# Performance work log

Hardware: AMD Instinct MI355X
Metric: run time of the kernel (lower is better)

## Reference

```python
import jax, jax.numpy as jnp
import numpy as np

B, S, D = 2, 2048, 4096
NH, NKV = 32, 8
HD = D // NH          # 128
NREP = NH // NKV      # 4 (GQA groups)


def _rope(t, cos, sin):
    # t: [b, s, h, d]; cos/sin: [s, d//2]; interleaved (real, imag) pairs on last dim
    tr = t.reshape(*t.shape[:-1], -1, 2)
    a, b = tr[..., 0], tr[..., 1]
    c = cos[None, :, None, :]
    s = sin[None, :, None, :]
    out = jnp.stack([a * c - b * s, a * s + b * c], axis=-1)
    return out.reshape(t.shape)


def _repeat_kv(t, n_rep):
    # [b, s, n_kv, d] -> [b, s, n_kv*n_rep, d]
    b, s, nkv, d = t.shape
    return jnp.broadcast_to(t[:, :, :, None, :], (b, s, nkv, n_rep, d)).reshape(b, s, nkv * n_rep, d)


def setup_inputs() -> dict:
    key = jax.random.key(0)
    ks = jax.random.split(key, 5)
    x = jax.random.normal(ks[0], (B, S, D), jnp.float32)
    wq = jax.random.normal(ks[1], (D, NH * HD), jnp.float32) * 0.02
    wk = jax.random.normal(ks[2], (D, NKV * HD), jnp.float32) * 0.02
    wv = jax.random.normal(ks[3], (D, NKV * HD), jnp.float32) * 0.02
    wo = jax.random.normal(ks[4], (NH * HD, D), jnp.float32) * 0.02
    inv_freq = 1.0 / (10000.0 ** (jnp.arange(0, HD, 2, dtype=jnp.float32) / HD))
    angles = jnp.arange(S, dtype=jnp.float32)[:, None] * inv_freq[None, :]  # [S, HD//2]
    return {
        "x": x, "wq": wq, "wk": wk, "wv": wv, "wo": wo,
        "freqs_cos": jnp.cos(angles), "freqs_sin": jnp.sin(angles),
        "start_pos": 0,
    }


def reference(x, wq, wk, wv, wo, freqs_cos, freqs_sin, start_pos):
    b, s, _ = x.shape
    xq = (x @ wq).reshape(b, s, NH, HD)
    xk = (x @ wk).reshape(b, s, NKV, HD)
    xv = (x @ wv).reshape(b, s, NKV, HD)
    xq = _rope(xq, freqs_cos, freqs_sin)
    xk = _rope(xk, freqs_cos, freqs_sin)
    # prefill (start_pos=0): cache[:b, :s] = xk/xv, then keys/values read back equal xk/xv
    keys = _repeat_kv(xk, NREP)    # [b, s, NH, HD]
    values = _repeat_kv(xv, NREP)  # [b, s, NH, HD]
    scores = jnp.einsum("bqhd,bkhd->bhqk", xq, keys) / jnp.sqrt(jnp.float32(HD))
    probs = jax.nn.softmax(scores, axis=-1)
    out = jnp.einsum("bhqk,bkhd->bqhd", probs, values).reshape(b, s, NH * HD)
    return out @ wo
```

## Files before the change

### kernel.cpp

```cpp
#include <hip/hip_runtime.h>
#include <hip/hip_bf16.h>
#include <cstdint>

#define B_   2
#define S_   2048
#define D_   4096
#define NH_  32
#define NKV_ 8
#define HD_  128
#define BS_  (B_*S_)
#define NQK_ 6144

typedef __bf16 bf16_t;
typedef __bf16 bf16x8 __attribute__((ext_vector_type(8)));
typedef __bf16 bf16x4 __attribute__((ext_vector_type(4)));
typedef __bf16 bf16x2 __attribute__((ext_vector_type(2)));
typedef float  f32x4  __attribute__((ext_vector_type(4)));
typedef unsigned uint32x4 __attribute__((ext_vector_type(4)));

typedef const __attribute__((address_space(1))) void* gas_ptr;
typedef __attribute__((address_space(3))) void* las_ptr;

__device__ __forceinline__ void gload_lds16(const void* g, void* l) {
  __builtin_amdgcn_global_load_lds((gas_ptr)g, (las_ptr)l, 16, 0, 0);
}

__device__ __forceinline__ float exp2_fast(float x) {
  float r;
  asm("v_exp_f32 %0, %1" : "=v"(r) : "v"(x));
  return r;
}

__device__ __forceinline__ unsigned cvt_pk_bf16(float a, float b) {
  unsigned r;
  asm("v_cvt_pk_bf16_f32 %0, %1, %2" : "=v"(r) : "v"(a), "v"(b));
  return r;
}

#define LD8(p) (*(const bf16x8*)(p))
#define MFMA(a, b, c) __builtin_amdgcn_mfma_f32_16x16x32_bf16(a, b, c, 0, 0, 0)

__global__ __launch_bounds__(256) void k_cvt(const float4* __restrict__ in,
                                             bf16x4* __restrict__ out, int n4) {
  int i = blockIdx.x * 256 + threadIdx.x;
  if (i >= n4) return;
  float4 v = in[i];
  bf16x4 o = { (bf16_t)v.x, (bf16_t)v.y, (bf16_t)v.z, (bf16_t)v.w };
  out[i] = o;
}

__global__ __launch_bounds__(256) void k_transpose_cvt(const float* __restrict__ w,
                                                       bf16_t* __restrict__ wt,
                                                       int K, int N) {
  __shared__ float tile[32][33];
  int n0 = blockIdx.x * 32, k0 = blockIdx.y * 32;
  int tx = threadIdx.x, ty = threadIdx.y;
#pragma unroll
  for (int i = 0; i < 4; i++)
    tile[ty + 8*i][tx] = w[(size_t)(k0 + ty + 8*i) * N + n0 + tx];
  __syncthreads();
#pragma unroll
  for (int i = 0; i < 4; i++)
    wt[(size_t)(n0 + ty + 8*i) * K + k0 + tx] = (bf16_t)tile[tx][ty + 8*i];
}

template <typename CT, int NF>
__global__ __launch_bounds__(512, 2) void k_gemm8p(const bf16_t* __restrict__ A,
                                                   const bf16_t* __restrict__ Bt,
                                                   CT* __restrict__ C,
                                                   int M, int N, int K) {
  __shared__ __align__(16) bf16_t As[2][256 * 64];
  __shared__ __align__(16) bf16_t Bs[2][NF * 64 * 64];
  const int tid = threadIdx.x;
  const int l = tid & 63, w = tid >> 6;
  const int lr = l & 15, lg = l >> 4;
  const int wm = w >> 2, wn = w & 3;

  const int bm = blockIdx.x, bn = blockIdx.y;

  const bf16_t* Ab = A  + (size_t)bm * 256 * K;
  const bf16_t* Bb = Bt + (size_t)bn * (NF * 64) * K;

  int st_row[4], st_col[4], st_dst[4];
#pragma unroll
  for (int j = 0; j < 4; j++) {
    int o = (j * 512 + tid) * 16;
    int row = o >> 7, cb = o & 127;
    st_row[j] = row;
    st_col[j] = (cb ^ ((row & 7) << 4)) >> 1;
    st_dst[j] = o >> 1;
  }

  int aoff[8], boff[NF];
#pragma unroll
  for (int m = 0; m < 8; m++) {
    int r = wm * 128 + m * 16 + lr;
    aoff[m] = r * 64 + (((lg * 16) ^ ((r & 7) << 4)) >> 1);
  }
#pragma unroll
  for (int n = 0; n < NF; n++) {
    int r = wn * (16 * NF) + n * 16 + lr;
    boff[n] = r * 64 + (((lg * 16) ^ ((r & 7) << 4)) >> 1);
  }

  f32x4 acc[8][NF];
#pragma unroll
  for (int m = 0; m < 8; m++)
#pragma unroll
    for (int n = 0; n < NF; n++) acc[m][n] = f32x4{0.f, 0.f, 0.f, 0.f};

  auto stageA = [&](int k, int h) {
    const int kt = k << 6;
    const int rof = h << 7;
#pragma unroll
    for (int j = 0; j < 2; j++)
      gload_lds16(Ab + (size_t)(st_row[j] + rof) * K + kt + st_col[j],
                  &As[k & 1][0] + (rof << 6) + st_dst[j]);
  };
  auto stageB = [&](int k) {
    const int kt = k << 6;
#pragma unroll
    for (int j = 0; j < NF; j++)
      gload_lds16(Bb + (size_t)st_row[j] * K + kt + st_col[j],
                  &Bs[k & 1][0] + st_dst[j]);
  };

  const int NT = K >> 6;
  stageA(0, 0); stageA(0, 1); stageB(0); stageB(1);
  if constexpr (NF == 3) asm volatile("s_waitcnt vmcnt(3)" ::: "memory");
  else                   asm volatile("s_waitcnt vmcnt(4)" ::: "memory");
  __builtin_amdgcn_s_barrier();

  for (int k = 0; k < NT; ++k) {
    const bf16_t* Ap = &As[k & 1][0];
    const bf16_t* Bp = &Bs[k & 1][0];
    const bool s1 = (k + 1 < NT), s2 = (k + 2 < NT);
    bf16x8 bfr[NF], a[4];

#pragma unroll
    for (int n = 0; n < NF; n++) bfr[n] = LD8(Bp + boff[n]);
#pragma unroll
    for (int m = 0; m < 4; m++) a[m] = LD8(Ap + aoff[m]);
    if (s1) stageA(k + 1, 0);
    __builtin_amdgcn_s_barrier();
    asm volatile("s_waitcnt lgkmcnt(0)" ::: "memory");
    __builtin_amdgcn_s_setprio(1);
#pragma unroll
    for (int m = 0; m < 4; m++)
#pragma unroll
      for (int n = 0; n < NF; n++)
        acc[m][n] = MFMA(a[m], bfr[n], acc[m][n]);
    __builtin_amdgcn_s_setprio(0);
    __builtin_amdgcn_s_barrier();

#pragma unroll
    for (int m = 0; m < 4; m++) a[m] = LD8(Ap + aoff[m + 4]);
    if (s1) stageA(k + 1, 1);
    __builtin_amdgcn_s_barrier();
    asm volatile("s_waitcnt lgkmcnt(0)" ::: "memory");
    __builtin_amdgcn_s_setprio(1);
#pragma unroll
    for (int m = 0; m < 4; m++)
#pragma unroll
      for (int n = 0; n < NF; n++)
        acc[m + 4][n] = MFMA(a[m], bfr[n], acc[m + 4][n]);
    __builtin_amdgcn_s_setprio(0);
    __builtin_amdgcn_s_barrier();

#pragma unroll
    for (int n = 0; n < NF; n++) bfr[n] = LD8(Bp + (boff[n] ^ 32));
#pragma unroll
    for (int m = 0; m < 4; m++) a[m] = LD8(Ap + (aoff[m] ^ 32));
    __builtin_amdgcn_s_barrier();
    asm volatile("s_waitcnt lgkmcnt(0)" ::: "memory");
    __builtin_amdgcn_s_setprio(1);
#pragma unroll
    for (int m = 0; m < 4; m++)
#pragma unroll
      for (int n = 0; n < NF; n++)
        acc[m][n] = MFMA(a[m], bfr[n], acc[m][n]);
    __builtin_amdgcn_s_setprio(0);
    __builtin_amdgcn_s_barrier();

#pragma unroll
    for (int m = 0; m < 4; m++) a[m] = LD8(Ap + (aoff[m + 4] ^ 32));
    if (s2) {
      stageB(k + 2);
      if constexpr (NF == 3) asm volatile("s_waitcnt vmcnt(3)" ::: "memory");
      else                   asm volatile("s_waitcnt vmcnt(4)" ::: "memory");
    } else if (s1) {
      asm volatile("s_waitcnt vmcnt(0)" ::: "memory");
    }
    __builtin_amdgcn_s_barrier();
    asm volatile("s_waitcnt lgkmcnt(0)" ::: "memory");
    __builtin_amdgcn_s_setprio(1);
#pragma unroll
    for (int m = 0; m < 4; m++)
#pragma unroll
      for (int n = 0; n < NF; n++)
        acc[m + 4][n] = MFMA(a[m], bfr[n], acc[m + 4][n]);
    __builtin_amdgcn_s_setprio(0);
    __builtin_amdgcn_s_barrier();
  }

#pragma unroll
  for (int m = 0; m < 8; m++) {
    int row0 = bm * 256 + wm * 128 + m * 16 + lg * 4;
#pragma unroll
    for (int n = 0; n < NF; n++) {
      int col = bn * (NF * 64) + wn * (16 * NF) + n * 16 + lr;
#pragma unroll
      for (int i = 0; i < 4; i++)
        C[(size_t)(row0 + i) * N + col] = (CT)acc[m][n][i];
    }
  }
}

__global__ __launch_bounds__(256) void k_rope(const bf16_t* __restrict__ qkv,
                                              const float* __restrict__ fcos,
                                              const float* __restrict__ fsin,
                                              bf16_t* __restrict__ dst,
                                              int nheads, int col_off, float mul) {
  int idx = blockIdx.x * 256 + threadIdx.x;
  int p = idx & 63;
  int h = (idx >> 6) % nheads;
  int bs = idx / (64 * nheads);
  int s = bs & (S_ - 1);
  int b = bs >> 11;
  const bf16_t* src = qkv + (size_t)bs * NQK_ + col_off + h * HD_ + 2 * p;
  bf16x2 ab = *(const bf16x2*)src;
  float a = (float)ab[0], bb = (float)ab[1];
  float c = fcos[s * 64 + p], sn = fsin[s * 64 + p];
  bf16x2 o = { (bf16_t)((a * c - bb * sn) * mul), (bf16_t)((a * sn + bb * c) * mul) };
  *(bf16x2*)(dst + ((((size_t)b * nheads + h) * S_ + s) * HD_) + 2 * p) = o;
}

__global__ __launch_bounds__(256) void k_vtrans(const bf16_t* __restrict__ qkv,
                                                bf16_t* __restrict__ vtr) {
  __shared__ bf16_t tile[32][33];
  int s0 = blockIdx.x * 32, d0 = blockIdx.y * 32, z = blockIdx.z;
  int b = z >> 3, kvh = z & 7;
  int tx = threadIdx.x, ty = threadIdx.y;
#pragma unroll
  for (int i = 0; i < 4; i++)
    tile[ty + 8*i][tx] =
        qkv[(size_t)(b * S_ + s0 + ty + 8*i) * NQK_ + (D_ + NKV_ * HD_) + kvh * HD_ + d0 + tx];
  __syncthreads();
#pragma unroll
  for (int i = 0; i < 4; i++)
    vtr[((size_t)z * HD_ + d0 + ty + 8*i) * S_ + s0 + tx] = tile[tx][ty + 8*i];
}

#define KVBLK 64
#define SM_THR 12.0f
__global__ __launch_bounds__(256, 2) void k_flash(const bf16_t* __restrict__ qr,
                                                  const bf16_t* __restrict__ kr,
                                                  const bf16_t* __restrict__ vt,
                                                  bf16_t* __restrict__ ctx) {
  __shared__ __align__(16) bf16_t Ks[2][KVBLK * HD_];
  __shared__ __align__(16) bf16_t Vs[2][HD_ * KVBLK];
  const int tid = threadIdx.x;
  const int l = tid & 63, w = tid >> 6;
  const int lr = l & 15, lg = l >> 4;
  const int qb = blockIdx.x, h = blockIdx.y, b = blockIdx.z;
  const int kvh = h >> 2;

  const bf16_t* qbase = qr + (((size_t)b * NH_ + h) * S_ + qb * 128 + w * 32) * HD_;
  const bf16_t* kbase = kr + (((size_t)b * NKV_ + kvh) * S_) * HD_;
  const bf16_t* vbase = vt + (((size_t)b * NKV_ + kvh) * HD_) * S_;

  const int sl0 = (lr + ((lg & 1) << 5)) << 2;
  const int sl1 = sl0 + (16 << 2);

  bf16x8 qf[2][4];
#pragma unroll
  for (int m = 0; m < 2; m++)
#pragma unroll
    for (int kk = 0; kk < 4; kk++)
      qf[m][kk] = *(const bf16x8*)(qbase + (m * 16 + lr) * HD_ + kk * 32 + lg * 8);

  bf16x8 ones;
#pragma unroll
  for (int j = 0; j < 8; j++) ones[j] = (bf16_t)1.0f;

  f32x4 o[2][9];
#pragma unroll
  for (int m = 0; m < 2; m++)
#pragma unroll
    for (int n = 0; n < 9; n++) o[m][n] = f32x4{0.f, 0.f, 0.f, 0.f};
  float mR[2] = {-1e30f, -1e30f};

  auto stage = [&](int bu, int t) {
    const int kb = t * KVBLK;
#pragma unroll
    for (int j = 0; j < 4; j++) {
      int o_ = (tid + 256 * j) * 16;
      int row = o_ >> 8, cb = o_ & 255;
      int scb = cb ^ ((row & 7) << 4);
      gload_lds16(kbase + (size_t)(kb + row) * HD_ + (scb >> 1),
                  &Ks[bu][0] + (o_ >> 1));
    }
#pragma unroll
    for (int j = 0; j < 4; j++) {
      int o_ = (tid + 256 * j) * 16;
      int row = o_ >> 7, cb = o_ & 127;
      int scb = cb ^ ((row & 7) << 4);
      gload_lds16(vbase + (size_t)row * S_ + kb + (scb >> 1),
                  &Vs[bu][0] + (o_ >> 1));
    }
  };

  const int nt = S_ / KVBLK;
  stage(0, 0);
  __syncthreads();
  int buf = 0;

  for (int t = 0; t < nt; t++) {
    if (t + 1 < nt) stage(buf ^ 1, t + 1);
    const bf16_t* Kb = &Ks[buf][0];
    const bf16_t* Vb = &Vs[buf][0];

    f32x4 sc[2][4];
#pragma unroll
    for (int m = 0; m < 2; m++)
#pragma unroll
      for (int n = 0; n < 4; n++) sc[m][n] = f32x4{0.f, 0.f, 0.f, 0.f};
    __builtin_amdgcn_s_setprio(1);
#pragma unroll
    for (int n = 0; n < 4; n++) {
#pragma unroll
      for (int kk = 0; kk < 4; kk++) {
        int r = n * 16 + lr;
        int cb = (kk * 64 + lg * 16) ^ ((r & 7) << 4);
        bf16x8 kf = *(const bf16x8*)(Kb + (((r << 8) + cb) >> 1));
        sc[0][n] = MFMA(kf, qf[0][kk], sc[0][n]);
        sc[1][n] = MFMA(kf, qf[1][kk], sc[1][n]);
      }
    }
    __builtin_amdgcn_s_setprio(0);

    bf16x8 pf[2][2];
#pragma unroll
    for (int m = 0; m < 2; m++) {
      float lm = sc[m][0][0];
#pragma unroll
      for (int n = 0; n < 4; n++)
#pragma unroll
        for (int i = 0; i < 4; i++)
          if (n | i) lm = fmaxf(lm, sc[m][n][i]);
      if (!__all(lm - mR[m] <= SM_THR)) {
        float tmx = fmaxf(lm, __shfl_xor(lm, 16));
        tmx = fmaxf(tmx, __shfl_xor(tmx, 32));
        float mnew = fmaxf(mR[m], tmx);
        float alpha = exp2_fast(mR[m] - mnew);
        mR[m] = mnew;
        float av[4];
#pragma unroll
        for (int i = 0; i < 4; i++) av[i] = __shfl(alpha, lg * 4 + i);
#pragma unroll
        for (int n = 0; n < 9; n++)
#pragma unroll
          for (int i = 0; i < 4; i++) o[m][n][i] *= av[i];
      }
      unsigned W[4][2];
#pragma unroll
      for (int n = 0; n < 4; n++) {
        float p0 = exp2_fast(sc[m][n][0] - mR[m]);
        float p1 = exp2_fast(sc[m][n][1] - mR[m]);
        float p2 = exp2_fast(sc[m][n][2] - mR[m]);
        float p3 = exp2_fast(sc[m][n][3] - mR[m]);
        W[n][0] = cvt_pk_bf16(p0, p1);
        W[n][1] = cvt_pk_bf16(p2, p3);
      }
#pragma unroll
      for (int kk = 0; kk < 2; kk++) {
        uint32x4 wv;
#pragma unroll
        for (int t = 0; t < 4; t++) {
          int srcb = (t < 2) ? sl0 : sl1;
          unsigned lo = (unsigned)__builtin_amdgcn_ds_bpermute(srcb, (int)W[2 * kk][t & 1]);
          unsigned hi = (unsigned)__builtin_amdgcn_ds_bpermute(srcb, (int)W[2 * kk + 1][t & 1]);
          wv[t] = (l & 32) ? hi : lo;
        }
        pf[m][kk] = __builtin_bit_cast(bf16x8, wv);
      }
    }

    __builtin_amdgcn_s_setprio(1);
#pragma unroll
    for (int n = 0; n < 8; n++) {
#pragma unroll
      for (int kk = 0; kk < 2; kk++) {
        int r = n * 16 + lr;
        int cb = (kk * 64 + lg * 16) ^ ((r & 7) << 4);
        bf16x8 vf = *(const bf16x8*)(Vb + (((r << 7) + cb) >> 1));
        o[0][n] = MFMA(pf[0][kk], vf, o[0][n]);
        o[1][n] = MFMA(pf[1][kk], vf, o[1][n]);
      }
    }
    o[0][8] = MFMA(pf[0][0], ones, o[0][8]);
    o[0][8] = MFMA(pf[0][1], ones, o[0][8]);
    o[1][8] = MFMA(pf[1][0], ones, o[1][8]);
    o[1][8] = MFMA(pf[1][1], ones, o[1][8]);
    __builtin_amdgcn_s_setprio(0);
    __syncthreads();
    buf ^= 1;
  }

#pragma unroll
  for (int m = 0; m < 2; m++)
#pragma unroll
    for (int i = 0; i < 4; i++) {
      float inv = 1.0f / o[m][8][i];
      int srow = qb * 128 + w * 32 + m * 16 + lg * 4 + i;
#pragma unroll
      for (int n = 0; n < 8; n++) {
        int d = n * 16 + lr;
        ctx[((size_t)(b * S_ + srow)) * D_ + h * HD_ + d] = (bf16_t)(o[m][n][i] * inv);
      }
    }
}

extern "C" void kernel_launch(void* const* d_in, const int* in_sizes, int n_in,
                              void* d_out, int out_size, void* d_ws, size_t ws_size,
                              hipStream_t stream) {
  const float* x    = (const float*)d_in[0];
  const float* wq   = (const float*)d_in[1];
  const float* wk   = (const float*)d_in[2];
  const float* wv   = (const float*)d_in[3];
  const float* wo   = (const float*)d_in[4];
  const float* fcos = (const float*)d_in[5];
  const float* fsin = (const float*)d_in[6];
  float* out = (float*)d_out;

  const size_t SZ_XB    = (size_t)BS_ * D_ * 2;
  const size_t SZ_WQKVT = (size_t)NQK_ * D_ * 2;
  const size_t SZ_WOT   = (size_t)D_ * D_ * 2;
  char* p = (char*)d_ws;
  bf16_t* xb    = (bf16_t*)p;
  bf16_t* wqkvt = (bf16_t*)(p + SZ_XB);
  bf16_t* wot   = (bf16_t*)(p + SZ_XB + SZ_WQKVT);
  bf16_t* qkv   = (bf16_t*)(p + SZ_XB + SZ_WQKVT + SZ_WOT);
  bf16_t* qrope = xb;
  bf16_t* krope = wqkvt;
  bf16_t* vtr   = wqkvt + (size_t)BS_ * NKV_ * HD_;
  bf16_t* ctx   = qkv;

  const float QSCALE = (float)(0.08838834764831845 * 1.4426950408889634);

  dim3 tb(32, 8);
  k_cvt<<<BS_ * D_ / 1024, 256, 0, stream>>>((const float4*)x, (bf16x4*)xb, BS_ * D_ / 4);
  k_transpose_cvt<<<dim3(D_ / 32, D_ / 32), tb, 0, stream>>>(wq, wqkvt, D_, D_);
  k_transpose_cvt<<<dim3(32, D_ / 32), tb, 0, stream>>>(wk, wqkvt + (size_t)D_ * D_, D_, NKV_ * HD_);
  k_transpose_cvt<<<dim3(32, D_ / 32), tb, 0, stream>>>(wv, wqkvt + (size_t)(D_ + NKV_ * HD_) * D_, D_, NKV_ * HD_);
  k_transpose_cvt<<<dim3(D_ / 32, D_ / 32), tb, 0, stream>>>(wo, wot, D_, D_);
  k_gemm8p<bf16_t, 3><<<dim3(BS_ / 256, NQK_ / 192), 512, 0, stream>>>(xb, wqkvt, qkv, BS_, NQK_, D_);
  k_rope<<<BS_ * NH_ * 64 / 256, 256, 0, stream>>>(qkv, fcos, fsin, qrope, NH_, 0, QSCALE);
  k_rope<<<BS_ * NKV_ * 64 / 256, 256, 0, stream>>>(qkv, fcos, fsin, krope, NKV_, D_, 1.0f);
  k_vtrans<<<dim3(S_ / 32, HD_ / 32, B_ * NKV_), tb, 0, stream>>>(qkv, vtr);
  k_flash<<<dim3(S_ / 128, NH_, B_), 256, 0, stream>>>(qrope, krope, vtr, ctx);
  k_gemm8p<float, 4><<<dim3(BS_ / 256, D_ / 256), 512, 0, stream>>>(ctx, wot, out, BS_, D_, D_);
}
```

Before: 606.0 us.

## Split QKV GEMM into Q GEMM and split-K KV GEMM with 256-wide tiles

The fused QKV projection with 192-wide N tiles becomes a Q-only GEMM plus a KV GEMM that uses split-K over two partial buffers. RoPE and V-transpose sum the two partials as they read them. The GEMM kernel now uses only the 256x256 (NF=4) tile. The intent is better tile efficiency and more blocks for the narrow KV part, since its 16x8 grid is too small to fill the GPU without split-K. In exchange it adds extra partial-buffer traffic and rounds the partial sums to bf16, and it reorders the wo transpose to reuse the workspace.

After: 575.1 us. 1.05x faster.

```diff
diff --git a/kernel.cpp b/kernel.cpp
--- a/kernel.cpp
+++ b/kernel.cpp
@@ -64,11 +64,13 @@
     wt[(size_t)(n0 + ty + 8*i) * K + k0 + tx] = (bf16_t)tile[tx][ty + 8*i];
 }
 
-template <typename CT, int NF>
+template <typename CT>
 __global__ __launch_bounds__(512, 2) void k_gemm8p(const bf16_t* __restrict__ A,
                                                    const bf16_t* __restrict__ Bt,
                                                    CT* __restrict__ C,
-                                                   int M, int N, int K) {
+                                                   int M, int N, int K, int KL,
+                                                   long long zsC) {
+  constexpr int NF = 4;
   __shared__ __align__(16) bf16_t As[2][256 * 64];
   __shared__ __align__(16) bf16_t Bs[2][NF * 64 * 64];
   const int tid = threadIdx.x;
@@ -77,9 +79,11 @@
   const int wm = w >> 2, wn = w & 3;
 
   const int bm = blockIdx.x, bn = blockIdx.y;
-
-  const bf16_t* Ab = A  + (size_t)bm * 256 * K;
-  const bf16_t* Bb = Bt + (size_t)bn * (NF * 64) * K;
+  const int kOff = blockIdx.z * KL;
+
+  const bf16_t* Ab = A  + (size_t)bm * 256 * K + kOff;
+  const bf16_t* Bb = Bt + (size_t)bn * 256 * K + kOff;
+  C += (long long)blockIdx.z * zsC;
 
   int st_row[4], st_col[4], st_dst[4];
 #pragma unroll
@@ -99,7 +103,7 @@
   }
 #pragma unroll
   for (int n = 0; n < NF; n++) {
-    int r = wn * (16 * NF) + n * 16 + lr;
+    int r = wn * 64 + n * 16 + lr;
     boff[n] = r * 64 + (((lg * 16) ^ ((r & 7) << 4)) >> 1);
   }
 
@@ -125,10 +129,9 @@
                   &Bs[k & 1][0] + st_dst[j]);
   };
 
-  const int NT = K >> 6;
+  const int NT = KL >> 6;
   stageA(0, 0); stageA(0, 1); stageB(0); stageB(1);
-  if constexpr (NF == 3) asm volatile("s_waitcnt vmcnt(3)" ::: "memory");
-  else                   asm volatile("s_waitcnt vmcnt(4)" ::: "memory");
+  asm volatile("s_waitcnt vmcnt(4)" ::: "memory");
   __builtin_amdgcn_s_barrier();
 
   for (int k = 0; k < NT; ++k) {
@@ -186,8 +189,7 @@
     for (int m = 0; m < 4; m++) a[m] = LD8(Ap + (aoff[m + 4] ^ 32));
     if (s2) {
       stageB(k + 2);
-      if constexpr (NF == 3) asm volatile("s_waitcnt vmcnt(3)" ::: "memory");
-      else                   asm volatile("s_waitcnt vmcnt(4)" ::: "memory");
+      asm volatile("s_waitcnt vmcnt(4)" ::: "memory");
     } else if (s1) {
       asm volatile("s_waitcnt vmcnt(0)" ::: "memory");
     }
@@ -208,7 +210,7 @@
     int row0 = bm * 256 + wm * 128 + m * 16 + lg * 4;
 #pragma unroll
     for (int n = 0; n < NF; n++) {
-      int col = bn * (NF * 64) + wn * (16 * NF) + n * 16 + lr;
+      int col = bn * 256 + wn * 64 + n * 16 + lr;
 #pragma unroll
       for (int i = 0; i < 4; i++)
         C[(size_t)(row0 + i) * N + col] = (CT)acc[m][n][i];
@@ -216,35 +218,42 @@
   }
 }
 
-__global__ __launch_bounds__(256) void k_rope(const bf16_t* __restrict__ qkv,
+__global__ __launch_bounds__(256) void k_rope(const bf16_t* __restrict__ s1,
+                                              const bf16_t* __restrict__ s2,
                                               const float* __restrict__ fcos,
                                               const float* __restrict__ fsin,
                                               bf16_t* __restrict__ dst,
-                                              int nheads, int col_off, float mul) {
+                                              int nheads, int stride, float mul) {
   int idx = blockIdx.x * 256 + threadIdx.x;
   int p = idx & 63;
   int h = (idx >> 6) % nheads;
   int bs = idx / (64 * nheads);
   int s = bs & (S_ - 1);
   int b = bs >> 11;
-  const bf16_t* src = qkv + (size_t)bs * NQK_ + col_off + h * HD_ + 2 * p;
-  bf16x2 ab = *(const bf16x2*)src;
+  size_t off = (size_t)bs * stride + h * HD_ + 2 * p;
+  bf16x2 ab = *(const bf16x2*)(s1 + off);
   float a = (float)ab[0], bb = (float)ab[1];
+  if (s2) {
+    bf16x2 ab2 = *(const bf16x2*)(s2 + off);
+    a += (float)ab2[0]; bb += (float)ab2[1];
+  }
   float c = fcos[s * 64 + p], sn = fsin[s * 64 + p];
   bf16x2 o = { (bf16_t)((a * c - bb * sn) * mul), (bf16_t)((a * sn + bb * c) * mul) };
   *(bf16x2*)(dst + ((((size_t)b * nheads + h) * S_ + s) * HD_) + 2 * p) = o;
 }
 
-__global__ __launch_bounds__(256) void k_vtrans(const bf16_t* __restrict__ qkv,
+__global__ __launch_bounds__(256) void k_vtrans(const bf16_t* __restrict__ pA,
+                                                const bf16_t* __restrict__ pB,
                                                 bf16_t* __restrict__ vtr) {
   __shared__ bf16_t tile[32][33];
   int s0 = blockIdx.x * 32, d0 = blockIdx.y * 32, z = blockIdx.z;
   int b = z >> 3, kvh = z & 7;
   int tx = threadIdx.x, ty = threadIdx.y;
 #pragma unroll
-  for (int i = 0; i < 4; i++)
-    tile[ty + 8*i][tx] =
-        qkv[(size_t)(b * S_ + s0 + ty + 8*i) * NQK_ + (D_ + NKV_ * HD_) + kvh * HD_ + d0 + tx];
+  for (int i = 0; i < 4; i++) {
+    size_t off = (size_t)(b * S_ + s0 + ty + 8*i) * 2048 + 1024 + kvh * HD_ + d0 + tx;
+    tile[ty + 8*i][tx] = (bf16_t)((float)pA[off] + (float)pB[off]);
+  }
   __syncthreads();
 #pragma unroll
   for (int i = 0; i < 4; i++)
@@ -376,11 +385,11 @@
       for (int kk = 0; kk < 2; kk++) {
         uint32x4 wv;
 #pragma unroll
-        for (int t = 0; t < 4; t++) {
-          int srcb = (t < 2) ? sl0 : sl1;
-          unsigned lo = (unsigned)__builtin_amdgcn_ds_bpermute(srcb, (int)W[2 * kk][t & 1]);
-          unsigned hi = (unsigned)__builtin_amdgcn_ds_bpermute(srcb, (int)W[2 * kk + 1][t & 1]);
-          wv[t] = (l & 32) ? hi : lo;
+        for (int t2 = 0; t2 < 4; t2++) {
+          int srcb = (t2 < 2) ? sl0 : sl1;
+          unsigned lo = (unsigned)__builtin_amdgcn_ds_bpermute(srcb, (int)W[2 * kk][t2 & 1]);
+          unsigned hi = (unsigned)__builtin_amdgcn_ds_bpermute(srcb, (int)W[2 * kk + 1][t2 & 1]);
+          wv[t2] = (l & 32) ? hi : lo;
         }
         pf[m][kk] = __builtin_bit_cast(bf16x8, wv);
       }
@@ -433,18 +442,18 @@
   const float* fsin = (const float*)d_in[6];
   float* out = (float*)d_out;
 
-  const size_t SZ_XB    = (size_t)BS_ * D_ * 2;
-  const size_t SZ_WQKVT = (size_t)NQK_ * D_ * 2;
-  const size_t SZ_WOT   = (size_t)D_ * D_ * 2;
+  const size_t MB = 1u << 20;
   char* p = (char*)d_ws;
   bf16_t* xb    = (bf16_t*)p;
-  bf16_t* wqkvt = (bf16_t*)(p + SZ_XB);
-  bf16_t* wot   = (bf16_t*)(p + SZ_XB + SZ_WQKVT);
-  bf16_t* qkv   = (bf16_t*)(p + SZ_XB + SZ_WQKVT + SZ_WOT);
+  bf16_t* wqkvt = (bf16_t*)(p + 32 * MB);
+  bf16_t* wot   = (bf16_t*)(p + 80 * MB);
+  bf16_t* qc    = (bf16_t*)(p + 112 * MB);
+  bf16_t* partA = (bf16_t*)(p + 144 * MB);
+  bf16_t* partB = wot;
   bf16_t* qrope = xb;
   bf16_t* krope = wqkvt;
   bf16_t* vtr   = wqkvt + (size_t)BS_ * NKV_ * HD_;
-  bf16_t* ctx   = qkv;
+  bf16_t* ctx   = qc;
 
   const float QSCALE = (float)(0.08838834764831845 * 1.4426950408889634);
 
@@ -453,11 +462,18 @@
   k_transpose_cvt<<<dim3(D_ / 32, D_ / 32), tb, 0, stream>>>(wq, wqkvt, D_, D_);
   k_transpose_cvt<<<dim3(32, D_ / 32), tb, 0, stream>>>(wk, wqkvt + (size_t)D_ * D_, D_, NKV_ * HD_);
   k_transpose_cvt<<<dim3(32, D_ / 32), tb, 0, stream>>>(wv, wqkvt + (size_t)(D_ + NKV_ * HD_) * D_, D_, NKV_ * HD_);
+  k_gemm8p<bf16_t><<<dim3(BS_ / 256, D_ / 256, 1), 512, 0, stream>>>(
+      xb, wqkvt, qc, BS_, D_, D_, D_, 0);
+  k_gemm8p<bf16_t><<<dim3(BS_ / 256, 2048 / 256, 2), 512, 0, stream>>>(
+      xb, wqkvt + (size_t)D_ * D_, partA, BS_, 2048, D_, 2048,
+      (long long)(partB - partA));
+  k_rope<<<BS_ * NH_ * 64 / 256, 256, 0, stream>>>(qc, (const bf16_t*)nullptr,
+      fcos, fsin, qrope, NH_, D_, QSCALE);
+  k_rope<<<BS_ * NKV_ * 64 / 256, 256, 0, stream>>>(partA, partB,
+      fcos, fsin, krope, NKV_, 2048, 1.0f);
+  k_vtrans<<<dim3(S_ / 32, HD_ / 32, B_ * NKV_), tb, 0, stream>>>(partA, partB, vtr);
   k_transpose_cvt<<<dim3(D_ / 32, D_ / 32), tb, 0, stream>>>(wo, wot, D_, D_);
-  k_gemm8p<bf16_t, 3><<<dim3(BS_ / 256, NQK_ / 192), 512, 0, stream>>>(xb, wqkvt, qkv, BS_, NQK_, D_);
-  k_rope<<<BS_ * NH_ * 64 / 256, 256, 0, stream>>>(qkv, fcos, fsin, qrope, NH_, 0, QSCALE);
-  k_rope<<<BS_ * NKV_ * 64 / 256, 256, 0, stream>>>(qkv, fcos, fsin, krope, NKV_, D_, 1.0f);
-  k_vtrans<<<dim3(S_ / 32, HD_ / 32, B_ * NKV_), tb, 0, stream>>>(qkv, vtr);
   k_flash<<<dim3(S_ / 128, NH_, B_), 256, 0, stream>>>(qrope, krope, vtr, ctx);
-  k_gemm8p<float, 4><<<dim3(BS_ / 256, D_ / 256), 512, 0, stream>>>(ctx, wot, out, BS_, D_, D_);
-}
+  k_gemm8p<float><<<dim3(BS_ / 256, D_ / 256, 1), 512, 0, stream>>>(
+      ctx, wot, out, BS_, D_, D_, D_, 0);
+}
```
